# Optimization experiments

Measured on AMD Instinct MI355X. Metric: run time of the kernel, lower is better.

Reference implementation:

```python
import jax, jax.numpy as jnp
import numpy as np

NAT, NN = 10000, 32
RSN, THETAN, NEMB = 16, 8, 4
RC = 5.0
ZETA = 16.0
FEAT = RSN * NEMB + RSN * THETAN * NEMB  # 576
PI = 3.141592653589793


def setup_inputs() -> dict:
    key = jax.random.key(0)
    ks = jax.random.split(key, 12)
    positions = jax.random.normal(ks[0], (NAT, 3), dtype=jnp.float32) * 2.0
    species_encoder = jax.random.normal(ks[1], (NAT, NEMB), dtype=jnp.float32)
    theta_s = jax.random.uniform(ks[2], (THETAN,), dtype=jnp.float32) * PI
    kn_rad = jnp.ones((1,), dtype=jnp.float32)
    neighbor_idx = jax.random.randint(ks[3], (NAT, NN), 0, NAT, dtype=jnp.int32)
    W1 = jax.random.normal(ks[4], (FEAT, 64), dtype=jnp.float32) / np.sqrt(FEAT)
    b1 = jnp.zeros((64,), dtype=jnp.float32)
    W2 = jax.random.normal(ks[5], (64, 64), dtype=jnp.float32) / 8.0
    b2 = jnp.zeros((64,), dtype=jnp.float32)
    W3 = jax.random.normal(ks[6], (64, 1), dtype=jnp.float32) / 8.0
    b3 = jnp.zeros((1,), dtype=jnp.float32)
    return {"positions": positions, "species_encoder": species_encoder,
            "theta_s": theta_s, "kn_rad": kn_rad,
            "W1": W1, "b1": b1, "W2": W2, "b2": b2, "W3": W3, "b3": b3,
            "neighbor_idx": neighbor_idx}


def _bessel_radial(rnorm, kn_rad):
    # spherical-Bessel radial basis with smooth cosine cutoff (help_fn.bessel_function)
    fc = 0.5 * (jnp.cos(PI * rnorm / RC) + 1.0) * (rnorm < RC).astype(rnorm.dtype)
    k = jnp.arange(1, RSN + 1, dtype=rnorm.dtype)                     # [RSN]
    arg = (PI / RC) * kn_rad[0] * k[None, None, :] * rnorm[..., None]  # [nat,NN,RSN]
    return jnp.sqrt(2.0 / RC) * jnp.sin(arg) / rnorm[..., None] * fc[..., None]


def reference(positions, species_encoder, theta_s, kn_rad,
              W1, b1, W2, b2, W3, b3, neighbor_idx):
    # gather neighbor displacements: [nat, NN, 3]
    rij = positions[neighbor_idx] - positions[:, None, :]
    rnorm = jnp.linalg.norm(rij, axis=-1) + 1e-8                      # [nat, NN]

    bf = _bessel_radial(rnorm, kn_rad)                                # [nat, NN, RSN]
    # center-x-neighbor species embedding product (einsum 'ijk->ik->ijk')
    semb_ij = species_encoder[neighbor_idx] * species_encoder[:, None, :]  # [nat,NN,NEMB]

    # radial descriptors: [nat, RSN, NEMB] -> [nat, RSN*NEMB]
    desc_rad = jnp.einsum('ijl,ijm->ilm', bf, semb_ij).reshape(NAT, -1)

    # angular part
    rij_unit = rij / rnorm[..., None]
    cos_ijk = jnp.einsum('ijc,ikc->ijk', rij_unit, rij_unit)          # [nat,NN,NN]
    cos_ijk = jnp.clip(cos_ijk, -1.0 + 1e-6, 1.0 - 1e-6)
    sin_ijk = jnp.sqrt(1.0 - cos_ijk * cos_ijk)
    ct, st = jnp.cos(theta_s), jnp.sin(theta_s)

    # factorized per-bond channel tensor P: [nat, NN, RSN*NEMB]
    P = jnp.einsum('ijl,ijm->ijlm', bf, semb_ij).reshape(NAT, NN, RSN * NEMB)
    pref = 2.0 ** (1.0 - ZETA)
    ang = []
    for t in range(THETAN):  # small fixed loop over angle centers
        cosd = cos_ijk * ct[t] + sin_ijk * st[t]                      # cos(theta - theta_s)
        A = pref * (1.0 + cosd) ** ZETA                               # [nat,NN,NN]
        C = jnp.einsum('ijk,ijp->ikp', A, P)                          # contract over j
        ang.append(jnp.sum(C * P, axis=1))                            # [nat, RSN*NEMB]
    desc_ang = jnp.stack(ang, axis=1).reshape(NAT, -1)                # [nat, THETAN*RSN*NEMB]

    desc = jnp.concatenate([desc_rad, desc_ang], axis=1)              # [nat, FEAT]

    # per-atom MLP -> atomic energies, scatter-sum to total energy
    h = jnp.tanh(desc @ W1 + b1)
    h = jnp.tanh(h @ W2 + b2)
    e_atom = (h @ W3 + b3)[:, 0]                                      # [nat]
    return jnp.sum(e_atom)
```

## Files before the change

### kernel.cpp

```cpp
#include <hip/hip_runtime.h>
#include <hip/hip_bf16.h>

#define NATC 10000
#define NATP 10016
#define NNC 32
#define RSNC 16
#define THETANC 8
#define NEMBC 4
#define FEATC 576

typedef __attribute__((ext_vector_type(8))) short short8;
typedef __attribute__((ext_vector_type(4))) float f32x4;
typedef __attribute__((ext_vector_type(2))) float f32x2;

static __device__ __forceinline__ short f2bf(float x) {
    union { __hip_bfloat16 h; short s; } u;
    u.h = __float2bfloat16(x);
    return u.s;
}

static __device__ __forceinline__ f32x2 pk_fma(f32x2 a, f32x2 b, f32x2 c) {
    f32x2 d;
    asm("v_pk_fma_f32 %0, %1, %2, %3" : "=v"(d) : "v"(a), "v"(b), "v"(c));
    return d;
}
static __device__ __forceinline__ f32x2 pk_mul(f32x2 a, f32x2 b) {
    f32x2 d;
    asm("v_pk_mul_f32 %0, %1, %2" : "=v"(d) : "v"(a), "v"(b));
    return d;
}
static __device__ __forceinline__ int cvt_pk_bf16(float lo, float hi) {
    int r;
    asm("v_cvt_pk_bf16_f32 %0, %1, %2" : "=v"(r) : "v"(lo), "v"(hi));
    return r;
}

static __device__ __forceinline__ int pow16_pair(f32x2 cv, f32x2 sv,
                                                 f32x2 tcv, f32x2 tsv, f32x2 sfv) {
    f32x2 y = pk_fma(cv, tcv, pk_fma(sv, tsv, sfv));
    y = pk_mul(y, y);
    y = pk_mul(y, y);
    y = pk_mul(y, y);
    y = pk_mul(y, y);
    return cvt_pk_bf16(y[0], y[1]);
}

__global__ __launch_bounds__(256, 5) void desc_kernel(
    const float* __restrict__ pos,
    const float* __restrict__ spe,
    const float* __restrict__ theta_s,
    const float* __restrict__ kn_rad,
    const int* __restrict__ nidx,
    ushort* __restrict__ descb,
    const float* __restrict__ W1, const float* __restrict__ W2,
    const float* __restrict__ b3,
    ushort* __restrict__ W1p, ushort* __restrict__ W2p,
    float* __restrict__ out)
{
    constexpr float RC = 5.0f;
    constexpr float PI_F = 3.14159265358979323846f;
    constexpr float SF = 0.52213689121f;

    const int tid = threadIdx.x;

    if (blockIdx.x >= NATC) {
        const int gid = (blockIdx.x - NATC) * 256 + tid;
        if (gid == 0) out[0] = (float)NATC * b3[0];
        if (gid < 4608) {
            const int l = gid & 63, ntks = gid >> 6;
            const int nt = ntks & 3, ks = ntks >> 2;
            const int qq = l >> 4, cc = l & 15;
            ushort pk[8];
            #pragma unroll
            for (int jj = 0; jj < 8; ++jj)
                pk[jj] = (ushort)f2bf(W1[(ks * 32 + qq * 8 + jj) * 64 + nt * 16 + cc]);
            #pragma unroll
            for (int jj = 0; jj < 8; ++jj) W1p[gid * 8 + jj] = pk[jj];
        } else {
            const int g = gid - 4608;
            const int l = g & 63, ntks = g >> 6;
            const int nt = ntks & 3, ks = ntks >> 2;
            const int qq = l >> 4, cc = l & 15;
            ushort pk[8];
            #pragma unroll
            for (int jj = 0; jj < 8; ++jj)
                pk[jj] = (ushort)f2bf(W2[(ks * 32 + qq * 8 + jj) * 64 + nt * 16 + cc]);
            #pragma unroll
            for (int jj = 0; jj < 8; ++jj) W2p[g * 8 + jj] = pk[jj];
        }
        return;
    }

    __shared__ __attribute__((aligned(16))) float Pt[64 * 36];
    __shared__ __attribute__((aligned(16))) float cosP[32 * 36];
    __shared__ __attribute__((aligned(16))) float sinP[32 * 36];
    __shared__ float thc[16];
    __shared__ float ux[32], uy[32], uz[32];
    __shared__ __attribute__((aligned(16))) float ses[32 * 5];
    __shared__ __attribute__((aligned(16))) float bfs[32 * 17];

    const int i = blockIdx.x;

    if (tid < NNC) {
        const int j = tid;
        const int n = nidx[i * NNC + j];
        const float pix = pos[i * 3 + 0], piy = pos[i * 3 + 1], piz = pos[i * 3 + 2];
        const float dx = pos[n * 3 + 0] - pix;
        const float dy = pos[n * 3 + 1] - piy;
        const float dz = pos[n * 3 + 2] - piz;
        const float r = sqrtf(dx * dx + dy * dy + dz * dz) + 1e-8f;
        const float inv = 1.0f / r;
        ux[j] = dx * inv; uy[j] = dy * inv; uz[j] = dz * inv;
        const float fc = (r < RC) ? 0.5f * (cosf(PI_F * r * (1.0f / RC)) + 1.0f) : 0.0f;
        const float rb = sqrtf(2.0f / RC) * inv * fc;
        const float x  = (PI_F / RC) * kn_rad[0] * r;
        float skm1 = sinf(x), skm2 = 0.0f;
        const float c2x = 2.0f * cosf(x);
        bfs[j * 17 + 0] = rb * skm1;
        #pragma unroll
        for (int k = 2; k <= 16; ++k) {
            const float sk = fmaf(c2x, skm1, -skm2);
            bfs[j * 17 + (k - 1)] = rb * sk;
            skm2 = skm1; skm1 = sk;
        }
        #pragma unroll
        for (int m = 0; m < NEMBC; ++m)
            ses[j * 5 + m] = spe[n * NEMBC + m] * spe[i * NEMBC + m];
    } else if (tid >= 64 && tid < 72) {
        const int t = tid - 64;
        const float th = theta_s[t];
        thc[2 * t]     = SF * cosf(th);
        thc[2 * t + 1] = SF * sinf(th);
    }
    __syncthreads();

    #pragma unroll
    for (int k = 0; k < 8; ++k) {
        const int e = tid + k * 256;
        const int j = e & 31, p = e >> 5;
        Pt[p * 36 + j] = bfs[j * 17 + (p >> 2)] * ses[j * 5 + (p & 3)];
    }
    #pragma unroll
    for (int k = 0; k < 4; ++k) {
        const int e = tid + k * 256;
        const int j = e & 31, kk = e >> 5;
        float cv = ux[j] * ux[kk] + uy[j] * uy[kk] + uz[j] * uz[kk];
        cv = fminf(fmaxf(cv, -1.0f + 1e-6f), 1.0f - 1e-6f);
        cosP[kk * 36 + j] = cv;
        sinP[kk * 36 + j] = sqrtf(fmaxf(1.0f - cv * cv, 0.0f));
    }
    __syncthreads();

    if (tid < 64) {
        const f32x4* pr = (const f32x4*)&Pt[tid * 36];
        float s = 0.0f;
        #pragma unroll
        for (int kb = 0; kb < 8; ++kb) {
            const f32x4 v = pr[kb];
            s += v[0]; s += v[1]; s += v[2]; s += v[3];
        }
        descb[(size_t)i * FEATC + tid] = (ushort)f2bf(s);
    }

    const int w = tid >> 6, l = tid & 63;
    const int q = l >> 4, c = l & 15;

    short8 pbr[4];
    #pragma unroll
    for (int nt = 0; nt < 4; ++nt) {
        const f32x4* prow = (const f32x4*)&Pt[(nt * 16 + c) * 36 + q * 8];
        const f32x4 p0 = prow[0], p1 = prow[1];
        union { short8 s8; int i4[4]; } u;
        u.i4[0] = cvt_pk_bf16(p0[0], p0[1]);
        u.i4[1] = cvt_pk_bf16(p0[2], p0[3]);
        u.i4[2] = cvt_pk_bf16(p1[0], p1[1]);
        u.i4[3] = cvt_pk_bf16(p1[2], p1[3]);
        pbr[nt] = u.s8;
    }

    #pragma unroll
    for (int tt = 0; tt < 2; ++tt) {
        const int t = w + tt * 4;
        const float tc = thc[2 * t], ts = thc[2 * t + 1];
        const f32x2 tcv = {tc, tc}, tsv = {ts, ts}, sfv = {SF, SF};

        short8 afr[2];
        #pragma unroll
        for (int mt = 0; mt < 2; ++mt) {
            const int kk = mt * 16 + c;
            const f32x4* cr = (const f32x4*)&cosP[kk * 36 + q * 8];
            const f32x4* sr = (const f32x4*)&sinP[kk * 36 + q * 8];
            const f32x4 c0 = cr[0], c1 = cr[1];
            const f32x4 s0 = sr[0], s1 = sr[1];
            union { short8 s8; int i4[4]; } u;
            u.i4[0] = pow16_pair((f32x2){c0[0], c0[1]}, (f32x2){s0[0], s0[1]}, tcv, tsv, sfv);
            u.i4[1] = pow16_pair((f32x2){c0[2], c0[3]}, (f32x2){s0[2], s0[3]}, tcv, tsv, sfv);
            u.i4[2] = pow16_pair((f32x2){c1[0], c1[1]}, (f32x2){s1[0], s1[1]}, tcv, tsv, sfv);
            u.i4[3] = pow16_pair((f32x2){c1[2], c1[3]}, (f32x2){s1[2], s1[3]}, tcv, tsv, sfv);
            afr[mt] = u.s8;
        }

        f32x4 acc[2][4];
        #pragma unroll
        for (int mt = 0; mt < 2; ++mt)
            #pragma unroll
            for (int nt = 0; nt < 4; ++nt)
                acc[mt][nt] = (f32x4){0.0f, 0.0f, 0.0f, 0.0f};

        #pragma unroll
        for (int nt = 0; nt < 4; ++nt) {
            acc[0][nt] = __builtin_amdgcn_mfma_f32_16x16x32_bf16(afr[0], pbr[nt], acc[0][nt], 0, 0, 0);
            acc[1][nt] = __builtin_amdgcn_mfma_f32_16x16x32_bf16(afr[1], pbr[nt], acc[1][nt], 0, 0, 0);
        }

        float ptv[4];
        #pragma unroll
        for (int nt = 0; nt < 4; ++nt) {
            f32x2 s2 = {0.0f, 0.0f};
            #pragma unroll
            for (int mt = 0; mt < 2; ++mt) {
                const f32x4 pv = *(const f32x4*)&Pt[(nt * 16 + c) * 36 + mt * 16 + q * 4];
                const f32x4 av = acc[mt][nt];
                s2 = pk_fma((f32x2){av[0], av[1]}, (f32x2){pv[0], pv[1]}, s2);
                s2 = pk_fma((f32x2){av[2], av[3]}, (f32x2){pv[2], pv[3]}, s2);
            }
            float s = s2[0] + s2[1];
            s += __shfl_xor(s, 16, 64);
            s += __shfl_xor(s, 32, 64);
            ptv[nt] = s;
        }
        const float v = (q == 0) ? ptv[0] : (q == 1) ? ptv[1] : (q == 2) ? ptv[2] : ptv[3];
        descb[(size_t)i * FEATC + 64 + t * 64 + l] = (ushort)f2bf(v);
    }
}

__global__ __launch_bounds__(256) void mlp_kernel(
    const ushort* __restrict__ descb,
    const ushort* __restrict__ W1p, const float* __restrict__ b1,
    const ushort* __restrict__ W2p, const float* __restrict__ b2,
    const float* __restrict__ W3,
    float* __restrict__ out)
{
    __shared__ __attribute__((aligned(16))) ushort H1b[16 * 72];
    __shared__ float red[4];

    const int tid = threadIdx.x;
    const int w = tid >> 6, l = tid & 63;
    const int q = l >> 4, c = l & 15;
    const int a0 = blockIdx.x * 16;

    f32x4 acc = (f32x4){0.0f, 0.0f, 0.0f, 0.0f};

    #pragma unroll 6
    for (int ks = 0; ks < 18; ++ks) {
        const short8 b   = *(const short8*)&W1p[((ks * 4 + w) * 64 + l) * 8];
        const short8 afr = *(const short8*)&descb[(size_t)(a0 + c) * FEATC + ks * 32 + q * 8];
        acc = __builtin_amdgcn_mfma_f32_16x16x32_bf16(afr, b, acc, 0, 0, 0);
    }

    const float b1v = b1[w * 16 + c];
    #pragma unroll
    for (int r = 0; r < 4; ++r)
        H1b[(q * 4 + r) * 72 + w * 16 + c] = (ushort)f2bf(tanhf(acc[r] + b1v));
    __syncthreads();

    f32x4 acc2 = (f32x4){0.0f, 0.0f, 0.0f, 0.0f};
    #pragma unroll
    for (int ks = 0; ks < 2; ++ks) {
        const short8 b   = *(const short8*)&W2p[((ks * 4 + w) * 64 + l) * 8];
        const short8 afr = *(const short8*)&H1b[c * 72 + ks * 32 + q * 8];
        acc2 = __builtin_amdgcn_mfma_f32_16x16x32_bf16(afr, b, acc2, 0, 0, 0);
    }

    const float b2v = b2[w * 16 + c];
    const float w3v = W3[w * 16 + c];
    float s = 0.0f;
    #pragma unroll
    for (int r = 0; r < 4; ++r) {
        const int a = a0 + q * 4 + r;
        if (a < NATC) s += tanhf(acc2[r] + b2v) * w3v;
    }
    #pragma unroll
    for (int off = 1; off <= 32; off <<= 1)
        s += __shfl_xor(s, off, 64);
    if (l == 0) red[w] = s;
    __syncthreads();
    if (tid == 0)
        atomicAdd(out, red[0] + red[1] + red[2] + red[3]);
}

extern "C" void kernel_launch(void* const* d_in, const int* in_sizes, int n_in,
                              void* d_out, int out_size, void* d_ws, size_t ws_size,
                              hipStream_t stream)
{
    const float* pos   = (const float*)d_in[0];
    const float* spe   = (const float*)d_in[1];
    const float* theta = (const float*)d_in[2];
    const float* kn    = (const float*)d_in[3];
    const float* W1    = (const float*)d_in[4];
    const float* b1    = (const float*)d_in[5];
    const float* W2    = (const float*)d_in[6];
    const float* b2    = (const float*)d_in[7];
    const float* W3    = (const float*)d_in[8];
    const float* b3    = (const float*)d_in[9];
    const int*   nidx  = (const int*)d_in[10];
    float* out = (float*)d_out;

    ushort* descb = (ushort*)d_ws;
    ushort* W1p   = (ushort*)((char*)d_ws + (size_t)NATP * FEATC * 2);
    ushort* W2p   = W1p + 4608 * 8;

    desc_kernel<<<NATC + 20, 256, 0, stream>>>(pos, spe, theta, kn, nidx, descb,
                                               W1, W2, b3, W1p, W2p, out);
    mlp_kernel<<<(NATC + 15) / 16, 256, 0, stream>>>(descb, W1p, b1, W2p, b2, W3, out);
}
```

Measured before the change: 132.3 us.

## Process two atoms per block and recompute sine terms in registers

Each block of the descriptor kernel now handles two atoms. Two waves serve each atom and each wave loops over four angle centers, so the grid is halved and per-block fixed costs like the shared-memory setup and the syncthreads are shared across more work. The sinP shared array is dropped and sin is recomputed from cos in registers just before the pow16 step. In exchange the kernel uses more shared memory, the occupancy hint drops from 5 to 4 blocks, and there are extra sqrt operations per angle center.

```diff
diff --git a/kernel.cpp b/kernel.cpp
--- a/kernel.cpp
+++ b/kernel.cpp
@@ -2,7 +2,7 @@
 #include <hip/hip_bf16.h>
 
 #define NATC 10000
-#define NATP 10016
+#define NATH 5000
 #define NNC 32
 #define RSNC 16
 #define THETANC 8
@@ -45,7 +45,7 @@
     return cvt_pk_bf16(y[0], y[1]);
 }
 
-__global__ __launch_bounds__(256, 5) void desc_kernel(
+__global__ __launch_bounds__(256, 4) void desc_kernel(
     const float* __restrict__ pos,
     const float* __restrict__ spe,
     const float* __restrict__ theta_s,
@@ -63,8 +63,8 @@
 
     const int tid = threadIdx.x;
 
-    if (blockIdx.x >= NATC) {
-        const int gid = (blockIdx.x - NATC) * 256 + tid;
+    if (blockIdx.x >= NATH) {
+        const int gid = (blockIdx.x - NATH) * 256 + tid;
         if (gid == 0) out[0] = (float)NATC * b3[0];
         if (gid < 4608) {
             const int l = gid & 63, ntks = gid >> 6;
@@ -91,18 +91,18 @@
         return;
     }
 
-    __shared__ __attribute__((aligned(16))) float Pt[64 * 36];
-    __shared__ __attribute__((aligned(16))) float cosP[32 * 36];
-    __shared__ __attribute__((aligned(16))) float sinP[32 * 36];
+    __shared__ __attribute__((aligned(16))) float Pt[2][64 * 36];
+    __shared__ __attribute__((aligned(16))) float cosP[2][32 * 36];
     __shared__ float thc[16];
-    __shared__ float ux[32], uy[32], uz[32];
-    __shared__ __attribute__((aligned(16))) float ses[32 * 5];
-    __shared__ __attribute__((aligned(16))) float bfs[32 * 17];
-
-    const int i = blockIdx.x;
-
-    if (tid < NNC) {
-        const int j = tid;
+    __shared__ float ux[2][32], uy[2][32], uz[2][32];
+    __shared__ __attribute__((aligned(16))) float ses[2][32 * 5];
+    __shared__ __attribute__((aligned(16))) float bfs[2][32 * 17];
+
+    const int i0 = blockIdx.x * 2;
+
+    if (tid < 64) {
+        const int a = tid >> 5, j = tid & 31;
+        const int i = i0 + a;
         const int n = nidx[i * NNC + j];
         const float pix = pos[i * 3 + 0], piy = pos[i * 3 + 1], piz = pos[i * 3 + 2];
         const float dx = pos[n * 3 + 0] - pix;
@@ -110,22 +110,22 @@
         const float dz = pos[n * 3 + 2] - piz;
         const float r = sqrtf(dx * dx + dy * dy + dz * dz) + 1e-8f;
         const float inv = 1.0f / r;
-        ux[j] = dx * inv; uy[j] = dy * inv; uz[j] = dz * inv;
+        ux[a][j] = dx * inv; uy[a][j] = dy * inv; uz[a][j] = dz * inv;
         const float fc = (r < RC) ? 0.5f * (cosf(PI_F * r * (1.0f / RC)) + 1.0f) : 0.0f;
         const float rb = sqrtf(2.0f / RC) * inv * fc;
         const float x  = (PI_F / RC) * kn_rad[0] * r;
         float skm1 = sinf(x), skm2 = 0.0f;
         const float c2x = 2.0f * cosf(x);
-        bfs[j * 17 + 0] = rb * skm1;
+        bfs[a][j * 17 + 0] = rb * skm1;
         #pragma unroll
         for (int k = 2; k <= 16; ++k) {
             const float sk = fmaf(c2x, skm1, -skm2);
-            bfs[j * 17 + (k - 1)] = rb * sk;
+            bfs[a][j * 17 + (k - 1)] = rb * sk;
             skm2 = skm1; skm1 = sk;
         }
         #pragma unroll
         for (int m = 0; m < NEMBC; ++m)
-            ses[j * 5 + m] = spe[n * NEMBC + m] * spe[i * NEMBC + m];
+            ses[a][j * 5 + m] = spe[n * NEMBC + m] * spe[i * NEMBC + m];
     } else if (tid >= 64 && tid < 72) {
         const int t = tid - 64;
         const float th = theta_s[t];
@@ -135,40 +135,44 @@
     __syncthreads();
 
     #pragma unroll
+    for (int k = 0; k < 16; ++k) {
+        const int e = tid + k * 256;
+        const int a = e >> 11, rem = e & 2047;
+        const int j = rem & 31, p = rem >> 5;
+        Pt[a][p * 36 + j] = bfs[a][j * 17 + (p >> 2)] * ses[a][j * 5 + (p & 3)];
+    }
+    #pragma unroll
     for (int k = 0; k < 8; ++k) {
         const int e = tid + k * 256;
-        const int j = e & 31, p = e >> 5;
-        Pt[p * 36 + j] = bfs[j * 17 + (p >> 2)] * ses[j * 5 + (p & 3)];
-    }
-    #pragma unroll
-    for (int k = 0; k < 4; ++k) {
-        const int e = tid + k * 256;
-        const int j = e & 31, kk = e >> 5;
-        float cv = ux[j] * ux[kk] + uy[j] * uy[kk] + uz[j] * uz[kk];
+        const int a = e >> 10, rem = e & 1023;
+        const int j = rem & 31, kk = rem >> 5;
+        float cv = ux[a][j] * ux[a][kk] + uy[a][j] * uy[a][kk] + uz[a][j] * uz[a][kk];
         cv = fminf(fmaxf(cv, -1.0f + 1e-6f), 1.0f - 1e-6f);
-        cosP[kk * 36 + j] = cv;
-        sinP[kk * 36 + j] = sqrtf(fmaxf(1.0f - cv * cv, 0.0f));
+        cosP[a][kk * 36 + j] = cv;
     }
     __syncthreads();
 
-    if (tid < 64) {
-        const f32x4* pr = (const f32x4*)&Pt[tid * 36];
+    if (tid < 128) {
+        const int a = tid >> 6, p = tid & 63;
+        const f32x4* pr = (const f32x4*)&Pt[a][p * 36];
         float s = 0.0f;
         #pragma unroll
         for (int kb = 0; kb < 8; ++kb) {
             const f32x4 v = pr[kb];
             s += v[0]; s += v[1]; s += v[2]; s += v[3];
         }
-        descb[(size_t)i * FEATC + tid] = (ushort)f2bf(s);
+        descb[(size_t)(i0 + a) * FEATC + p] = (ushort)f2bf(s);
     }
 
     const int w = tid >> 6, l = tid & 63;
     const int q = l >> 4, c = l & 15;
+    const int a = w >> 1, wl = w & 1;
+    const int i = i0 + a;
 
     short8 pbr[4];
     #pragma unroll
     for (int nt = 0; nt < 4; ++nt) {
-        const f32x4* prow = (const f32x4*)&Pt[(nt * 16 + c) * 36 + q * 8];
+        const f32x4* prow = (const f32x4*)&Pt[a][(nt * 16 + c) * 36 + q * 8];
         const f32x4 p0 = prow[0], p1 = prow[1];
         union { short8 s8; int i4[4]; } u;
         u.i4[0] = cvt_pk_bf16(p0[0], p0[1]);
@@ -178,9 +182,8 @@
         pbr[nt] = u.s8;
     }
 
-    #pragma unroll
-    for (int tt = 0; tt < 2; ++tt) {
-        const int t = w + tt * 4;
+    for (int tt = 0; tt < 4; ++tt) {
+        const int t = wl * 4 + tt;
         const float tc = thc[2 * t], ts = thc[2 * t + 1];
         const f32x2 tcv = {tc, tc}, tsv = {ts, ts}, sfv = {SF, SF};
 
@@ -188,15 +191,21 @@
         #pragma unroll
         for (int mt = 0; mt < 2; ++mt) {
             const int kk = mt * 16 + c;
-            const f32x4* cr = (const f32x4*)&cosP[kk * 36 + q * 8];
-            const f32x4* sr = (const f32x4*)&sinP[kk * 36 + q * 8];
+            const f32x4* cr = (const f32x4*)&cosP[a][kk * 36 + q * 8];
             const f32x4 c0 = cr[0], c1 = cr[1];
-            const f32x4 s0 = sr[0], s1 = sr[1];
+            const float sv0 = sqrtf(fmaxf(1.0f - c0[0] * c0[0], 0.0f));
+            const float sv1 = sqrtf(fmaxf(1.0f - c0[1] * c0[1], 0.0f));
+            const float sv2 = sqrtf(fmaxf(1.0f - c0[2] * c0[2], 0.0f));
+            const float sv3 = sqrtf(fmaxf(1.0f - c0[3] * c0[3], 0.0f));
+            const float sv4 = sqrtf(fmaxf(1.0f - c1[0] * c1[0], 0.0f));
+            const float sv5 = sqrtf(fmaxf(1.0f - c1[1] * c1[1], 0.0f));
+            const float sv6 = sqrtf(fmaxf(1.0f - c1[2] * c1[2], 0.0f));
+            const float sv7 = sqrtf(fmaxf(1.0f - c1[3] * c1[3], 0.0f));
             union { short8 s8; int i4[4]; } u;
-            u.i4[0] = pow16_pair((f32x2){c0[0], c0[1]}, (f32x2){s0[0], s0[1]}, tcv, tsv, sfv);
-            u.i4[1] = pow16_pair((f32x2){c0[2], c0[3]}, (f32x2){s0[2], s0[3]}, tcv, tsv, sfv);
-            u.i4[2] = pow16_pair((f32x2){c1[0], c1[1]}, (f32x2){s1[0], s1[1]}, tcv, tsv, sfv);
-            u.i4[3] = pow16_pair((f32x2){c1[2], c1[3]}, (f32x2){s1[2], s1[3]}, tcv, tsv, sfv);
+            u.i4[0] = pow16_pair((f32x2){c0[0], c0[1]}, (f32x2){sv0, sv1}, tcv, tsv, sfv);
+            u.i4[1] = pow16_pair((f32x2){c0[2], c0[3]}, (f32x2){sv2, sv3}, tcv, tsv, sfv);
+            u.i4[2] = pow16_pair((f32x2){c1[0], c1[1]}, (f32x2){sv4, sv5}, tcv, tsv, sfv);
+            u.i4[3] = pow16_pair((f32x2){c1[2], c1[3]}, (f32x2){sv6, sv7}, tcv, tsv, sfv);
             afr[mt] = u.s8;
         }
 
@@ -219,10 +228,10 @@
             f32x2 s2 = {0.0f, 0.0f};
             #pragma unroll
             for (int mt = 0; mt < 2; ++mt) {
-                const f32x4 pv = *(const f32x4*)&Pt[(nt * 16 + c) * 36 + mt * 16 + q * 4];
+                const f32x4 pvv = *(const f32x4*)&Pt[a][(nt * 16 + c) * 36 + mt * 16 + q * 4];
                 const f32x4 av = acc[mt][nt];
-                s2 = pk_fma((f32x2){av[0], av[1]}, (f32x2){pv[0], pv[1]}, s2);
-                s2 = pk_fma((f32x2){av[2], av[3]}, (f32x2){pv[2], pv[3]}, s2);
+                s2 = pk_fma((f32x2){av[0], av[1]}, (f32x2){pvv[0], pvv[1]}, s2);
+                s2 = pk_fma((f32x2){av[2], av[3]}, (f32x2){pvv[2], pvv[3]}, s2);
             }
             float s = s2[0] + s2[1];
             s += __shfl_xor(s, 16, 64);
@@ -307,10 +316,10 @@
     float* out = (float*)d_out;
 
     ushort* descb = (ushort*)d_ws;
-    ushort* W1p   = (ushort*)((char*)d_ws + (size_t)NATP * FEATC * 2);
+    ushort* W1p   = (ushort*)((char*)d_ws + (size_t)(NATC + 16) * FEATC * 2);
     ushort* W2p   = W1p + 4608 * 8;
 
-    desc_kernel<<<NATC + 20, 256, 0, stream>>>(pos, spe, theta, kn, nidx, descb,
+    desc_kernel<<<NATH + 20, 256, 0, stream>>>(pos, spe, theta, kn, nidx, descb,
                                                W1, W2, b3, W1p, W2p, out);
     mlp_kernel<<<(NATC + 15) / 16, 256, 0, stream>>>(descb, W1p, b1, W2p, b2, W3, out);
 }
```

After: 147.9 us. 11.8% more time.
